# Optimization experiments

Measured on AMD Instinct MI355X. Metric: run time of the kernel, lower is better.

The kernel has to match this reference:

```python
import jax, jax.numpy as jnp
import numpy as np

N_NODES = 100000
N_EDGES = 1200000
IN_DIM = 64
OUT_DIM = 64


def setup_inputs() -> dict:
    key = jax.random.key(0)
    k1, k2, k3, k4, k5 = jax.random.split(key, 5)
    x = jax.random.normal(k1, (N_NODES, IN_DIM), dtype=jnp.float32)
    src = jax.random.randint(k2, (N_EDGES,), 0, N_NODES, dtype=jnp.int32)
    dst = jax.random.randint(k3, (N_EDGES,), 0, N_NODES, dtype=jnp.int32)
    # nn.Linear(in_dim, out_dim): weight [out, in], bias [out]
    bound = 1.0 / np.sqrt(IN_DIM)
    W = jax.random.uniform(k4, (OUT_DIM, IN_DIM), minval=-bound, maxval=bound, dtype=jnp.float32)
    b = jax.random.uniform(k5, (OUT_DIM,), minval=-bound, maxval=bound, dtype=jnp.float32)
    return {"x": x, "src": src, "dst": dst, "W": W, "b": b}


def reference(x, src, dst, W, b):
    # copy_u('h','m') + mean('m','h_neigh'): per-destination mean of source features
    msg_sum = jax.ops.segment_sum(x[src], dst, num_segments=N_NODES)  # [N, in_dim]
    deg = jax.ops.segment_sum(jnp.ones_like(dst, dtype=x.dtype), dst, num_segments=N_NODES)
    h = msg_sum / jnp.maximum(deg, 1.0)[:, None]  # isolated nodes -> 0 (DGL mean semantics)
    # linear: h @ W^T + b
    return h @ W.T + b
```

## Files before the change

### kernel.cpp

```cpp
#include <hip/hip_runtime.h>

#define N_NODES 100000
#define N_EDGES 1200000
#define DIM 64
#define NPW 8
#define WPB 4


__global__ __launch_bounds__(256, 8) void hist_rank_kernel(
    const int* __restrict__ dst, int* __restrict__ counts,
    int* __restrict__ rank, int n2)
{
    int i = blockIdx.x * blockDim.x + threadIdx.x;
    if (i >= n2) return;
    int2 d = ((const int2*)dst)[i];
    int r0 = atomicAdd(&counts[d.x], 1);
    int r1 = atomicAdd(&counts[d.y], 1);
    ((int2*)rank)[i] = make_int2(r0, r1);
}

__global__ __launch_bounds__(256) void offsets_kernel(
    const int* __restrict__ counts, int* __restrict__ offsets,
    int* __restrict__ base_counter, int n)
{
    __shared__ int tmp[256];
    __shared__ int base;
    int i = blockIdx.x * 256 + threadIdx.x;
    int v = (i < n) ? counts[i] : 0;
    tmp[threadIdx.x] = v;
    __syncthreads();
    #pragma unroll
    for (int d = 1; d < 256; d <<= 1) {
        int t = (threadIdx.x >= d) ? tmp[threadIdx.x - d] : 0;
        __syncthreads();
        tmp[threadIdx.x] += t;
        __syncthreads();
    }
    if (threadIdx.x == 255) base = atomicAdd(base_counter, tmp[255]);
    __syncthreads();
    if (i < n) offsets[i] = base + tmp[threadIdx.x] - v;
}

__global__ __launch_bounds__(256, 8) void fill_kernel(
    const int* __restrict__ src, const int* __restrict__ dst,
    const int* __restrict__ rank, const int* __restrict__ offsets,
    int* __restrict__ csr_src, int n2)
{
    int i = blockIdx.x * blockDim.x + threadIdx.x;
    if (i >= n2) return;
    int2 s = ((const int2*)src)[i];
    int2 d = ((const int2*)dst)[i];
    int2 r = ((const int2*)rank)[i];
    csr_src[offsets[d.x] + r.x] = s.x;
    csr_src[offsets[d.y] + r.y] = s.y;
}

__global__ __launch_bounds__(256) void aggregate_linear_kernel(
    const float* __restrict__ x, const int* __restrict__ csr_src,
    const int* __restrict__ offsets, const int* __restrict__ counts,
    const float* __restrict__ W, const float* __restrict__ bias,
    float* __restrict__ out, int n_nodes)
{
    __shared__ float Ws[DIM][68];
    __shared__ float hs[WPB][DIM];

    for (int i = threadIdx.x; i < DIM * DIM / 4; i += 256) {
        float4 wv = ((const float4*)W)[i];
        int o = i >> 4, fq = i & 15;
        *(float4*)&Ws[o][fq * 4] = wv;
    }
    __syncthreads();

    int w    = threadIdx.x >> 6;
    int lane = threadIdx.x & 63;
    int g    = lane >> 4;
    int gl   = lane & 15;
    float bl = bias[lane];

    int node0 = (blockIdx.x * WPB + w) * NPW;
    #pragma unroll 1
    for (int ni = 0; ni < NPW; ++ni) {
        int node = node0 + ni;
        if (node >= n_nodes) break;

        int off = offsets[node];
        int deg = counts[node];
        int end = off + deg;
        float4 a0 = {0.f, 0.f, 0.f, 0.f};
        float4 a1 = {0.f, 0.f, 0.f, 0.f};
        for (int k = off; k < end; k += 8) {
            int e0 = k + g, e1 = k + 4 + g;
            int s0 = csr_src[min(e0, end - 1)];
            int s1 = csr_src[min(e1, end - 1)];
            float4 v0 = *(const float4*)&x[(size_t)s0 * DIM + gl * 4];
            float4 v1 = *(const float4*)&x[(size_t)s1 * DIM + gl * 4];
            bool p0 = e0 < end, p1 = e1 < end;
            a0.x += p0 ? v0.x : 0.f;  a0.y += p0 ? v0.y : 0.f;
            a0.z += p0 ? v0.z : 0.f;  a0.w += p0 ? v0.w : 0.f;
            a1.x += p1 ? v1.x : 0.f;  a1.y += p1 ? v1.y : 0.f;
            a1.z += p1 ? v1.z : 0.f;  a1.w += p1 ? v1.w : 0.f;
        }
        a0.x += a1.x; a0.y += a1.y; a0.z += a1.z; a0.w += a1.w;
        a0.x += __shfl_xor(a0.x, 16, 64); a0.x += __shfl_xor(a0.x, 32, 64);
        a0.y += __shfl_xor(a0.y, 16, 64); a0.y += __shfl_xor(a0.y, 32, 64);
        a0.z += __shfl_xor(a0.z, 16, 64); a0.z += __shfl_xor(a0.z, 32, 64);
        a0.w += __shfl_xor(a0.w, 16, 64); a0.w += __shfl_xor(a0.w, 32, 64);

        float inv = 1.0f / fmaxf((float)deg, 1.0f);
        if (g == 0) {
            float4 h4 = {a0.x * inv, a0.y * inv, a0.z * inv, a0.w * inv};
            *(float4*)&hs[w][gl * 4] = h4;
        }
        __builtin_amdgcn_wave_barrier();

        float acc = bl;
        #pragma unroll
        for (int f0 = 0; f0 < DIM; f0 += 4) {
            float4 hv = *(const float4*)&hs[w][f0];
            float4 wv = *(const float4*)&Ws[lane][f0];
            acc = fmaf(hv.x, wv.x, acc);
            acc = fmaf(hv.y, wv.y, acc);
            acc = fmaf(hv.z, wv.z, acc);
            acc = fmaf(hv.w, wv.w, acc);
        }
        __builtin_nontemporal_store(acc, &out[(size_t)node * DIM + lane]);
        __builtin_amdgcn_wave_barrier();
    }
}

extern "C" void kernel_launch(void* const* d_in, const int* in_sizes, int n_in,
                              void* d_out, int out_size, void* d_ws, size_t ws_size,
                              hipStream_t stream) {
    const float* x   = (const float*)d_in[0];
    const int*   src = (const int*)d_in[1];
    const int*   dst = (const int*)d_in[2];
    const float* W   = (const float*)d_in[3];
    const float* b   = (const float*)d_in[4];
    float* out = (float*)d_out;

    int* counts       = (int*)d_ws;
    int* base_counter = counts + 100032;
    int* offsets      = base_counter + 32;
    int* rank         = offsets + 100032;
    int* csr_src      = rank + N_EDGES;

    hipMemsetAsync(counts, 0, (size_t)(100032 + 32) * sizeof(int), stream);

    int n2 = N_EDGES / 2;
    int eb2 = (n2 + 255) / 256;
    int nb = (N_NODES + 255) / 256;

    hist_rank_kernel<<<eb2, 256, 0, stream>>>(dst, counts, rank, n2);
    offsets_kernel  <<<nb, 256, 0, stream>>>(counts, offsets, base_counter, N_NODES);
    fill_kernel     <<<eb2, 256, 0, stream>>>(src, dst, rank, offsets, csr_src, n2);

    int blocks = (N_NODES + WPB * NPW - 1) / (WPB * NPW);
    aggregate_linear_kernel<<<blocks, 256, 0, stream>>>(
        x, csr_src, offsets, counts, W, b, out, N_NODES);
}
```

Measured before the change: 214.5 us.

## Apply linear transform before aggregation and overlap GEMM with histogram

Uses linearity to compute y = xW^T per node first, then aggregates y by destination and adds bias after the mean. The per-node GEMM runs in the same launch as the degree histogram, in separate block ranges, so compute overlaps with the atomic-bound histogram. The aggregation kernel no longer does the per-node matvec and no longer loads W into shared memory. This adds a full N×64 intermediate write and read, and falls back to the old path if the workspace is too small.

```diff
diff --git a/kernel.cpp b/kernel.cpp
--- a/kernel.cpp
+++ b/kernel.cpp
@@ -5,9 +5,53 @@
 #define DIM 64
 #define NPW 8
 #define WPB 4
-
-
-__global__ __launch_bounds__(256, 8) void hist_rank_kernel(
+#define HB 1536
+#define GB 1536
+
+__global__ __launch_bounds__(256) void hist_gemm_kernel(
+    const int* __restrict__ dst, int* __restrict__ counts, int* __restrict__ rank,
+    const float* __restrict__ x, const float* __restrict__ W,
+    float* __restrict__ y, int n2, int n_nodes)
+{
+    if (blockIdx.x < HB) {
+        for (int i = blockIdx.x * 256 + threadIdx.x; i < n2; i += HB * 256) {
+            int2 d = ((const int2*)dst)[i];
+            int r0 = atomicAdd(&counts[d.x], 1);
+            int r1 = atomicAdd(&counts[d.y], 1);
+            ((int2*)rank)[i] = make_int2(r0, r1);
+        }
+    } else {
+        __shared__ float Ws[DIM][68];
+        __shared__ float hs[WPB][DIM];
+        for (int i = threadIdx.x; i < DIM * DIM / 4; i += 256) {
+            float4 wv = ((const float4*)W)[i];
+            *(float4*)&Ws[i >> 4][(i & 15) * 4] = wv;
+        }
+        __syncthreads();
+        int w = threadIdx.x >> 6, lane = threadIdx.x & 63;
+        int wave_id = (blockIdx.x - HB) * WPB + w;
+        for (int node = wave_id; node < n_nodes; node += GB * WPB) {
+            hs[w][lane] = x[(size_t)node * DIM + lane];
+            __builtin_amdgcn_wave_barrier();
+            float acc0 = 0.f, acc1 = 0.f;
+            #pragma unroll
+            for (int f0 = 0; f0 < DIM; f0 += 8) {
+                float4 h0 = *(const float4*)&hs[w][f0];
+                float4 h1 = *(const float4*)&hs[w][f0 + 4];
+                float4 w0 = *(const float4*)&Ws[lane][f0];
+                float4 w1 = *(const float4*)&Ws[lane][f0 + 4];
+                acc0 = fmaf(h0.x, w0.x, acc0); acc0 = fmaf(h0.y, w0.y, acc0);
+                acc0 = fmaf(h0.z, w0.z, acc0); acc0 = fmaf(h0.w, w0.w, acc0);
+                acc1 = fmaf(h1.x, w1.x, acc1); acc1 = fmaf(h1.y, w1.y, acc1);
+                acc1 = fmaf(h1.z, w1.z, acc1); acc1 = fmaf(h1.w, w1.w, acc1);
+            }
+            y[(size_t)node * DIM + lane] = acc0 + acc1;
+            __builtin_amdgcn_wave_barrier();
+        }
+    }
+}
+
+__global__ __launch_bounds__(256) void hist_rank_kernel(
     const int* __restrict__ dst, int* __restrict__ counts,
     int* __restrict__ rank, int n2)
 {
@@ -41,7 +85,7 @@
     if (i < n) offsets[i] = base + tmp[threadIdx.x] - v;
 }
 
-__global__ __launch_bounds__(256, 8) void fill_kernel(
+__global__ __launch_bounds__(256) void fill_kernel(
     const int* __restrict__ src, const int* __restrict__ dst,
     const int* __restrict__ rank, const int* __restrict__ offsets,
     int* __restrict__ csr_src, int n2)
@@ -55,6 +99,55 @@
     csr_src[offsets[d.y] + r.y] = s.y;
 }
 
+__global__ __launch_bounds__(256) void aggregate_y_kernel(
+    const float* __restrict__ y, const int* __restrict__ csr_src,
+    const int* __restrict__ offsets, const int* __restrict__ counts,
+    const float* __restrict__ bias, float* __restrict__ out, int n_nodes)
+{
+    int w    = threadIdx.x >> 6;
+    int lane = threadIdx.x & 63;
+    int g    = lane >> 4;
+    int gl   = lane & 15;
+    float4 b4 = ((const float4*)bias)[gl];
+
+    int node0 = (blockIdx.x * WPB + w) * NPW;
+    #pragma unroll 1
+    for (int ni = 0; ni < NPW; ++ni) {
+        int node = node0 + ni;
+        if (node >= n_nodes) break;
+
+        int off = offsets[node];
+        int deg = counts[node];
+        int end = off + deg;
+        float4 a0 = {0.f, 0.f, 0.f, 0.f};
+        float4 a1 = {0.f, 0.f, 0.f, 0.f};
+        for (int k = off; k < end; k += 8) {
+            int e0 = k + g, e1 = k + 4 + g;
+            int s0 = csr_src[min(e0, end - 1)];
+            int s1 = csr_src[min(e1, end - 1)];
+            float4 v0 = *(const float4*)&y[(size_t)s0 * DIM + gl * 4];
+            float4 v1 = *(const float4*)&y[(size_t)s1 * DIM + gl * 4];
+            bool p0 = e0 < end, p1 = e1 < end;
+            a0.x += p0 ? v0.x : 0.f;  a0.y += p0 ? v0.y : 0.f;
+            a0.z += p0 ? v0.z : 0.f;  a0.w += p0 ? v0.w : 0.f;
+            a1.x += p1 ? v1.x : 0.f;  a1.y += p1 ? v1.y : 0.f;
+            a1.z += p1 ? v1.z : 0.f;  a1.w += p1 ? v1.w : 0.f;
+        }
+        a0.x += a1.x; a0.y += a1.y; a0.z += a1.z; a0.w += a1.w;
+        a0.x += __shfl_xor(a0.x, 16, 64); a0.x += __shfl_xor(a0.x, 32, 64);
+        a0.y += __shfl_xor(a0.y, 16, 64); a0.y += __shfl_xor(a0.y, 32, 64);
+        a0.z += __shfl_xor(a0.z, 16, 64); a0.z += __shfl_xor(a0.z, 32, 64);
+        a0.w += __shfl_xor(a0.w, 16, 64); a0.w += __shfl_xor(a0.w, 32, 64);
+
+        if (g == 0) {
+            float inv = 1.0f / fmaxf((float)deg, 1.0f);
+            float4 o4 = {fmaf(a0.x, inv, b4.x), fmaf(a0.y, inv, b4.y),
+                         fmaf(a0.z, inv, b4.z), fmaf(a0.w, inv, b4.w)};
+            *(float4*)&out[(size_t)node * DIM + gl * 4] = o4;
+        }
+    }
+}
+
 __global__ __launch_bounds__(256) void aggregate_linear_kernel(
     const float* __restrict__ x, const int* __restrict__ csr_src,
     const int* __restrict__ offsets, const int* __restrict__ counts,
@@ -63,26 +156,19 @@
 {
     __shared__ float Ws[DIM][68];
     __shared__ float hs[WPB][DIM];
-
     for (int i = threadIdx.x; i < DIM * DIM / 4; i += 256) {
         float4 wv = ((const float4*)W)[i];
-        int o = i >> 4, fq = i & 15;
-        *(float4*)&Ws[o][fq * 4] = wv;
+        *(float4*)&Ws[i >> 4][(i & 15) * 4] = wv;
     }
     __syncthreads();
-
-    int w    = threadIdx.x >> 6;
-    int lane = threadIdx.x & 63;
-    int g    = lane >> 4;
-    int gl   = lane & 15;
+    int w = threadIdx.x >> 6, lane = threadIdx.x & 63;
+    int g = lane >> 4, gl = lane & 15;
     float bl = bias[lane];
-
     int node0 = (blockIdx.x * WPB + w) * NPW;
     #pragma unroll 1
     for (int ni = 0; ni < NPW; ++ni) {
         int node = node0 + ni;
         if (node >= n_nodes) break;
-
         int off = offsets[node];
         int deg = counts[node];
         int end = off + deg;
@@ -105,14 +191,12 @@
         a0.y += __shfl_xor(a0.y, 16, 64); a0.y += __shfl_xor(a0.y, 32, 64);
         a0.z += __shfl_xor(a0.z, 16, 64); a0.z += __shfl_xor(a0.z, 32, 64);
         a0.w += __shfl_xor(a0.w, 16, 64); a0.w += __shfl_xor(a0.w, 32, 64);
-
         float inv = 1.0f / fmaxf((float)deg, 1.0f);
         if (g == 0) {
             float4 h4 = {a0.x * inv, a0.y * inv, a0.z * inv, a0.w * inv};
             *(float4*)&hs[w][gl * 4] = h4;
         }
         __builtin_amdgcn_wave_barrier();
-
         float acc = bl;
         #pragma unroll
         for (int f0 = 0; f0 < DIM; f0 += 4) {
@@ -143,18 +227,30 @@
     int* offsets      = base_counter + 32;
     int* rank         = offsets + 100032;
     int* csr_src      = rank + N_EDGES;
+    float* y          = (float*)(csr_src + N_EDGES);
+
+    size_t need = (size_t)(100032 + 32 + 100032 + 2 * N_EDGES) * 4
+                + (size_t)N_NODES * DIM * 4;
 
     hipMemsetAsync(counts, 0, (size_t)(100032 + 32) * sizeof(int), stream);
 
     int n2 = N_EDGES / 2;
     int eb2 = (n2 + 255) / 256;
     int nb = (N_NODES + 255) / 256;
-
-    hist_rank_kernel<<<eb2, 256, 0, stream>>>(dst, counts, rank, n2);
-    offsets_kernel  <<<nb, 256, 0, stream>>>(counts, offsets, base_counter, N_NODES);
-    fill_kernel     <<<eb2, 256, 0, stream>>>(src, dst, rank, offsets, csr_src, n2);
-
-    int blocks = (N_NODES + WPB * NPW - 1) / (WPB * NPW);
-    aggregate_linear_kernel<<<blocks, 256, 0, stream>>>(
-        x, csr_src, offsets, counts, W, b, out, N_NODES);
-}
+    int ablocks = (N_NODES + WPB * NPW - 1) / (WPB * NPW);
+
+    if (ws_size >= need) {
+        hist_gemm_kernel<<<HB + GB, 256, 0, stream>>>(dst, counts, rank, x, W, y,
+                                                      n2, N_NODES);
+        offsets_kernel  <<<nb, 256, 0, stream>>>(counts, offsets, base_counter, N_NODES);
+        fill_kernel     <<<eb2, 256, 0, stream>>>(src, dst, rank, offsets, csr_src, n2);
+        aggregate_y_kernel<<<ablocks, 256, 0, stream>>>(y, csr_src, offsets, counts,
+                                                        b, out, N_NODES);
+    } else {
+        hist_rank_kernel<<<eb2, 256, 0, stream>>>(dst, counts, rank, n2);
+        offsets_kernel  <<<nb, 256, 0, stream>>>(counts, offsets, base_counter, N_NODES);
+        fill_kernel     <<<eb2, 256, 0, stream>>>(src, dst, rank, offsets, csr_src, n2);
+        aggregate_linear_kernel<<<ablocks, 256, 0, stream>>>(x, csr_src, offsets,
+                                                             counts, W, b, out, N_NODES);
+    }
+}
```

After: 257.9 us. +20.2%, slower.
